# Kernel optimization log

Measured on AMD Instinct MI355X. Metric: run time of the kernel, lower is better.

Reference implementation:

```python
import jax, jax.numpy as jnp
import numpy as np

B, CIN, COUT, CH, H, W = 8, 3, 1, 64, 256, 256
MODES, LAYERS = 4, 6


def conv1x1(x, w, b):
    # x: (B,C,H,W), w: (O,C), b: (O,)
    return jnp.einsum('bchw,oc->bohw', x, w) + b[None, :, None, None]


def koopman(x, w1, w2):
    # FNO-style spectral conv: rfft2 -> truncated-mode complex multiply -> irfft2
    m = MODES
    xf = jnp.fft.rfft2(x)                                    # (B,C,H,W//2+1) complex
    o1 = jnp.einsum('bixy,ioxy->boxy', xf[:, :, :m, :m], w1)
    o2 = jnp.einsum('bixy,ioxy->boxy', xf[:, :, -m:, :m], w2)
    of = jnp.zeros(xf.shape, dtype=xf.dtype)
    of = of.at[:, :, :m, :m].set(o1)
    of = of.at[:, :, -m:, :m].set(o2)
    return jnp.fft.irfft2(of, s=(H, W))


def setup_inputs() -> dict:
    key = jax.random.key(0)
    ks = jax.random.split(key, 12)
    scale = 1.0 / (CH * CH)
    inp = {
        'x': jax.random.normal(ks[0], (B, CIN, H, W), dtype=jnp.float32),
        'enc_w': jax.random.normal(ks[1], (CH, CIN), dtype=jnp.float32) * (1.0 / np.sqrt(CIN)),
        'enc_b': jax.random.normal(ks[2], (CH,), dtype=jnp.float32) * 0.01,
        'dec1_w': jax.random.normal(ks[3], (CH, CH), dtype=jnp.float32) * (1.0 / np.sqrt(CH)),
        'dec1_b': jax.random.normal(ks[4], (CH,), dtype=jnp.float32) * 0.01,
        'dec2_w': jax.random.normal(ks[5], (COUT, CH), dtype=jnp.float32) * (1.0 / np.sqrt(CH)),
        'dec2_b': jax.random.normal(ks[6], (COUT,), dtype=jnp.float32) * 0.01,
        'w1r': jax.random.uniform(ks[7], (CH, CH, MODES, MODES), dtype=jnp.float32) * scale,
        'w1i': jax.random.uniform(ks[8], (CH, CH, MODES, MODES), dtype=jnp.float32) * scale,
        'w2r': jax.random.uniform(ks[9], (CH, CH, MODES, MODES), dtype=jnp.float32) * scale,
        'w2i': jax.random.uniform(ks[10], (CH, CH, MODES, MODES), dtype=jnp.float32) * scale,
    }
    return inp


def reference(x, enc_w, enc_b, dec1_w, dec1_b, dec2_w, dec2_b, w1r, w1i, w2r, w2i):
    w1 = w1r + 1j * w1i
    w2 = w2r + 1j * w2i
    h = jnp.tanh(conv1x1(x, enc_w, enc_b))          # encoder
    skip = h
    for _ in range(LAYERS):                         # fixed small layer count
        h = h + koopman(h, w1, w2)
    h = h + skip
    h = jnp.tanh(conv1x1(h, dec1_w, dec1_b))        # decoder
    return conv1x1(h, dec2_w, dec2_b)
```

## Files before the change

kernel.cpp:

```cpp
#include <hip/hip_runtime.h>
#include <hip/hip_bf16.h>

#define NB 8
#define NCIN 3
#define NCH 64
#define NH 256
#define NW 256
#define NM 4
#define NLAYERS 6

typedef short s16x8 __attribute__((ext_vector_type(8)));
typedef float f32x4 __attribute__((ext_vector_type(4)));

__device__ __forceinline__ float fast_tanh(float x) {
    float e = __expf(2.0f * x);
    return 1.0f - 2.0f * __builtin_amdgcn_rcpf(1.0f + e);
}
__device__ __forceinline__ float sin2pi(float x) { return __builtin_amdgcn_sinf(x); }
__device__ __forceinline__ float cos2pi(float x) { return __builtin_amdgcn_cosf(x); }

__device__ __forceinline__ unsigned int pk2(float a, float b) {
    __hip_bfloat162 h = __float22bfloat162_rn(make_float2(a, b));
    unsigned int u; __builtin_memcpy(&u, &h, 4); return u;
}
__device__ __forceinline__ s16x8 u4cast(uint4 u) {
    s16x8 r; __builtin_memcpy(&r, &u, 16); return r;
}
__device__ __forceinline__ unsigned short f2bf(float f) {
    unsigned int u = __float_as_uint(f);
    u = u + 0x7fffu + ((u >> 16) & 1u);
    return (unsigned short)(u >> 16);
}

__global__ __launch_bounds__(256) void k_prep(
    const float* __restrict__ dec1_w, const float* __restrict__ enc_w,
    const float* __restrict__ enc_b,
    const float* __restrict__ w1r, const float* __restrict__ w1i,
    const float* __restrict__ w2r, const float* __restrict__ w2i,
    unsigned short* __restrict__ Wpk, unsigned short* __restrict__ Tpk,
    float* __restrict__ encwb, float* __restrict__ Wtr, float* __restrict__ Wti,
    float* __restrict__ d1wT)
{
    const int bid = blockIdx.x;
    const int t   = threadIdx.x;
    if (bid < 1024) {
        int elem = bid * 256 + t;
        int ri = elem >> 17;
        int rem = elem & 0x1FFFF;
        int p  = rem >> 14;
        int q  = (rem >> 12) & 3;
        int i  = (rem >> 6) & 63;
        int o  = rem & 63;
        const float* src;
        if (p < 4) src = ri ? w1i : w1r;
        else       src = ri ? w2i : w2r;
        float v = src[((i * 64 + o) * 4 + (p & 3)) * 4 + q];
        float* dst = ri ? Wti : Wtr;
        dst[(p * 4 + q) * 4096 + i * 64 + o] = v;
    } else if (bid < 1026) {
        const int tt = (bid - 1024) * 256 + t;
        const int o  = tt & 63;
        const int cb = (tt >> 6) * 8;
        const float* wr = dec1_w + o * NCH + cb;
        float4 wa = ((const float4*)wr)[0];
        float4 wb = ((const float4*)wr)[1];
        float v[8] = {wa.x, wa.y, wa.z, wa.w, wb.x, wb.y, wb.z, wb.w};
        unsigned int ph[4], pl[4];
        #pragma unroll
        for (int j = 0; j < 4; ++j) {
            unsigned int h = pk2(v[2 * j], v[2 * j + 1]);
            float ha = __uint_as_float(h << 16);
            float hb = __uint_as_float(h & 0xffff0000u);
            ph[j] = h;
            pl[j] = pk2(v[2 * j] - ha, v[2 * j + 1] - hb);
        }
        int byteoff = (o * 128 + cb * 2) ^ ((o & 7) << 4);
        *(uint4*)((char*)Wpk + byteoff)        = make_uint4(ph[0], ph[1], ph[2], ph[3]);
        *(uint4*)((char*)Wpk + 8192 + byteoff) = make_uint4(pl[0], pl[1], pl[2], pl[3]);
    } else if (bid < 1030) {
        const int tt = (bid - 1026) * 256 + t;
        const int n  = tt >> 6;
        const int w4 = (tt & 63) * 4;
        float vv[4];
        #pragma unroll
        for (int z = 0; z < 4; ++z) {
            int w = w4 + z;
            float val = 0.f;
            if (n < 4)      val = cos2pi((float)(n * w) * (1.0f / 256.0f));
            else if (n < 8) val = -sin2pi((float)((n - 4) * w) * (1.0f / 256.0f));
            vv[z] = val;
        }
        *(uint2*)(Tpk + n * 256 + w4) = make_uint2(pk2(vv[0], vv[1]), pk2(vv[2], vv[3]));
    } else if (bid == 1030) {
        if (t < NCH) {
            float4 e4;
            e4.x = enc_w[t * 3 + 0]; e4.y = enc_w[t * 3 + 1];
            e4.z = enc_w[t * 3 + 2]; e4.w = enc_b[t];
            ((float4*)encwb)[t] = e4;
        }
    } else {
        for (int idx = t; idx < 4096; idx += 256) {
            int c = idx >> 6, o = idx & 63;
            d1wT[idx] = dec1_w[o * NCH + c];
        }
    }
}

__global__ __launch_bounds__(256) void k_enc_mfma(
    const float* __restrict__ x, const float* __restrict__ encwb,
    const unsigned short* __restrict__ Tpk, float* __restrict__ P2)
{
    __shared__ __align__(16) unsigned short Ah[64 * 128];
    const int bi  = blockIdx.x;
    const int b   = bi >> 9;
    const int rem = bi & 511;
    const int row = rem >> 1;
    const int wh  = rem & 1;
    const int t   = threadIdx.x;

    {
        const int c   = t & 63;
        const int wl0 = (t >> 6) * 32;
        float4 ewb = ((const float4*)encwb)[c];
        const float* xr0 = x + ((b * 3 + 0) * NH + row) * NW + wh * 128 + wl0;
        const float* xr1 = x + ((b * 3 + 1) * NH + row) * NW + wh * 128 + wl0;
        const float* xr2 = x + ((b * 3 + 2) * NH + row) * NW + wh * 128 + wl0;
        #pragma unroll
        for (int u = 0; u < 4; ++u) {
            float4 a0 = ((const float4*)xr0)[u * 2], b0 = ((const float4*)xr0)[u * 2 + 1];
            float4 a1 = ((const float4*)xr1)[u * 2], b1 = ((const float4*)xr1)[u * 2 + 1];
            float4 a2 = ((const float4*)xr2)[u * 2], b2 = ((const float4*)xr2)[u * 2 + 1];
            float hv[8];
            hv[0] = fast_tanh(ewb.w + ewb.x * a0.x + ewb.y * a1.x + ewb.z * a2.x);
            hv[1] = fast_tanh(ewb.w + ewb.x * a0.y + ewb.y * a1.y + ewb.z * a2.y);
            hv[2] = fast_tanh(ewb.w + ewb.x * a0.z + ewb.y * a1.z + ewb.z * a2.z);
            hv[3] = fast_tanh(ewb.w + ewb.x * a0.w + ewb.y * a1.w + ewb.z * a2.w);
            hv[4] = fast_tanh(ewb.w + ewb.x * b0.x + ewb.y * b1.x + ewb.z * b2.x);
            hv[5] = fast_tanh(ewb.w + ewb.x * b0.y + ewb.y * b1.y + ewb.z * b2.y);
            hv[6] = fast_tanh(ewb.w + ewb.x * b0.z + ewb.y * b1.z + ewb.z * b2.z);
            hv[7] = fast_tanh(ewb.w + ewb.x * b0.w + ewb.y * b1.w + ewb.z * b2.w);
            uint4 pu = make_uint4(pk2(hv[0], hv[1]), pk2(hv[2], hv[3]),
                                  pk2(hv[4], hv[5]), pk2(hv[6], hv[7]));
            int byteoff = (c * 256 + (wl0 + u * 8) * 2) ^ ((c & 15) << 4);
            *(uint4*)((char*)Ah + byteoff) = pu;
        }
    }
    __syncthreads();

    const int lane = t & 63;
    const int v    = t >> 6;
    const int li   = lane & 15;
    const int g    = lane >> 4;
    f32x4 acc = {0.f, 0.f, 0.f, 0.f};
    #pragma unroll
    for (int kk = 0; kk < 4; ++kk) {
        int cm = v * 16 + li;
        int coff = (cm * 256 + (kk * 32 + g * 8) * 2) ^ ((cm & 15) << 4);
        s16x8 ah = *(const s16x8*)((const char*)Ah + coff);
        int wg = wh * 128 + kk * 32 + g * 8;
        s16x8 bh = *(const s16x8*)(Tpk + li * 256 + wg);
        acc = __builtin_amdgcn_mfma_f32_16x16x32_bf16(ah, bh, acc, 0, 0, 0);
    }
    if (li < 8) {
        const int q = li & 3, reim = li >> 2;
        float* pbase = P2 + (size_t)wh * (NB * 64 * 256 * 8);
        #pragma unroll
        for (int e = 0; e < 4; ++e) {
            int c = v * 16 + g * 4 + e;
            pbase[(((b * 64 + c) * 256 + row) * 4 + q) * 2 + reim] = acc[e];
        }
    }
}

__global__ __launch_bounds__(64) void k_coldft(const float* __restrict__ P2,
                                               float2* __restrict__ s0)
{
    __shared__ __align__(16) float Ps[256][8];
    __shared__ float twc[5][256];
    __shared__ float tws[5][256];
    const int b = blockIdx.x >> 6;
    const int c = blockIdx.x & 63;
    const int t = threadIdx.x;
    {
        const float4* pa = (const float4*)(P2 + (size_t)(b * 64 + c) * 256 * 8);
        const float4* pb = pa + (size_t)NB * 64 * 256 * 2;
        float4* ds = (float4*)&Ps[0][0];
        #pragma unroll
        for (int k = 0; k < 8; ++k) {
            int s = t + 64 * k;
            float4 u = pa[s], v = pb[s];
            ds[s] = make_float4(u.x + v.x, u.y + v.y, u.z + v.z, u.w + v.w);
        }
        for (int idx = t; idx < 5 * 256; idx += 64) {
            int k = idx >> 8, rw = idx & 255;
            float a = (float)(k * rw) * (1.0f / 256.0f);
            twc[k][rw] = cos2pi(a);
            tws[k][rw] = sin2pi(a);
        }
    }
    __syncthreads();
    const int kxs[8] = {0, 1, 2, 3, -4, -3, -2, -1};
    const int p = t >> 3, q = (t >> 1) & 3, reim = t & 1;
    const int kx = kxs[p];
    const int ka = kx < 0 ? -kx : kx;
    const float sgn = (kx < 0) ? 1.f : -1.f;
    float acc = 0.f;
    #pragma unroll 4
    for (int rw = 0; rw < 256; ++rw) {
        float pr = Ps[rw][q * 2], pi = Ps[rw][q * 2 + 1];
        float tr = twc[ka][rw], ti = sgn * tws[ka][rw];
        acc += reim ? (pr * ti + pi * tr) : (pr * tr - pi * ti);
    }
    ((float*)s0)[(((b * 8 + p) * 4 + q) * NCH + c) * 2 + reim] = acc;
}

__global__ __launch_bounds__(128) void k_spec(
    const float* __restrict__ Wtr, const float* __restrict__ Wti,
    const float* __restrict__ d1wT, const float2* __restrict__ s0,
    float2* __restrict__ dd2)
{
    __shared__ float Wr[2][NCH * NCH];
    __shared__ float Wi[2][NCH * NCH];
    __shared__ float sr[2][NCH], si[2][NCH];
    __shared__ float2 FL[2][NCH];
    __shared__ float W1T[NCH * NCH];
    const int gx    = blockIdx.x;
    const int b     = gx / 17;
    const int slot  = gx % 17;
    const int which = threadIdx.x >> 6;
    const int o     = threadIdx.x & 63;
    const int tid   = threadIdx.x;

    int p = -1, q = 0, g = -1;
    if (slot < 12) {
        int r = slot * 2 + which;
        q = (r >> 3) + 1;
        p = r & 7;
    } else {
        g = slot - 12;
        if (which == 0) p = g;
        else            p = (g == 1) ? 7 : (g == 2) ? 6 : (g == 3) ? 5 : -1;
        q = 0;
    }
    const bool active = (p >= 0);

    if (active) {
        const float4* wr = (const float4*)(Wtr + (p * 4 + q) * 4096);
        const float4* wi = (const float4*)(Wti + (p * 4 + q) * 4096);
        float4* dr = (float4*)&Wr[which][0];
        float4* di = (float4*)&Wi[which][0];
        #pragma unroll
        for (int k = 0; k < 16; ++k) {
            dr[o + 64 * k] = wr[o + 64 * k];
            di[o + 64 * k] = wi[o + 64 * k];
        }
        float2 sv = s0[((b * 8 + p) * 4 + q) * NCH + o];
        sr[which][o] = sv.x; si[which][o] = sv.y;
    }
    {
        float4* w1 = (float4*)W1T;
        const float4* sw = (const float4*)d1wT;
        #pragma unroll
        for (int k = 0; k < 8; ++k) w1[tid + 128 * k] = sw[tid + 128 * k];
    }
    __syncthreads();

    float dr = 0.f, di = 0.f, d8r = 0.f, d8i = 0.f;
    if (slot < 12) {
        for (int l = 0; l < NLAYERS; ++l) {
            float Fr = 0.f, Fi = 0.f;
            for (int i = 0; i < NCH; ++i) {
                float a0 = sr[which][i], a1 = si[which][i];
                float b0 = Wr[which][i * NCH + o], b1 = Wi[which][i * NCH + o];
                Fr += a0 * b0 - a1 * b1;
                Fi += a0 * b1 + a1 * b0;
            }
            __syncthreads();
            sr[which][o] += Fr; si[which][o] += Fi;
            dr += Fr; di += Fi;
            __syncthreads();
        }
    } else {
        for (int l = 0; l < NLAYERS; ++l) {
            float Fr = 0.f, Fi = 0.f;
            if (active) {
                for (int i = 0; i < NCH; ++i) {
                    float a0 = sr[which][i], a1 = si[which][i];
                    float b0 = Wr[which][i * NCH + o], b1 = Wi[which][i * NCH + o];
                    Fr += a0 * b0 - a1 * b1;
                    Fi += a0 * b1 + a1 * b0;
                }
            }
            FL[which][o] = make_float2(Fr, Fi);
            __syncthreads();
            float addr_ = 0.f, addi_ = 0.f;
            if (active) {
                if (g == 0) { addr_ = Fr; addi_ = 0.f; }
                else if (g == 4) {
                    addr_ = 0.5f * Fr; addi_ = 0.5f * Fi;
                    d8r += 0.5f * Fr;  d8i -= 0.5f * Fi;
                } else {
                    float2 Fo = FL[1 - which][o];
                    addr_ = 0.5f * (Fr + Fo.x);
                    addi_ = 0.5f * (Fi - Fo.y);
                }
                sr[which][o] += addr_; si[which][o] += addi_;
                dr += addr_; di += addi_;
            }
            __syncthreads();
        }
    }

    sr[which][o] = dr; si[which][o] = di;
    if (slot == 16 && which == 0) FL[0][o] = make_float2(d8r, d8i);
    __syncthreads();
    float2* db = dd2 + (size_t)b * (9 * 4 * NCH);
    if (active) {
        float ar = 0.f, ai = 0.f;
        for (int c = 0; c < NCH; ++c) {
            float wv = W1T[c * NCH + o];
            ar += sr[which][c] * wv;
            ai += si[which][c] * wv;
        }
        db[(p * 4 + q) * NCH + o] = make_float2(ar, ai);
    }
    if (slot == 16 && which == 0) {
        float ar = 0.f, ai = 0.f;
        for (int c = 0; c < NCH; ++c) {
            float wv = W1T[c * NCH + o];
            ar += FL[0][c].x * wv;
            ai += FL[0][c].y * wv;
        }
        db[(8 * 4 + 0) * NCH + o] = make_float2(ar, ai);
    }
}

__global__ __launch_bounds__(256) void k_final(
    const float* __restrict__ x, const float* __restrict__ encwb,
    const unsigned short* __restrict__ Wpk, const float2* __restrict__ dd2,
    const float* __restrict__ dec1_b, const float* __restrict__ dec2_w,
    const float* __restrict__ dec2_b, float* __restrict__ out)
{
    __shared__ __align__(16) unsigned short Wl[2][NCH * NCH];
    __shared__ __align__(16) unsigned short BcsT[NCH][8];
    const int bi   = blockIdx.x;
    const int b    = bi >> 9;
    const int rem  = bi & 511;
    const int row  = rem >> 1;
    const int half = rem & 1;
    const int t    = threadIdx.x;

    {
        const uint4* src = (const uint4*)Wpk;
        uint4* dst = (uint4*)&Wl[0][0];
        #pragma unroll
        for (int k = 0; k < 4; ++k) dst[t + 256 * k] = src[t + 256 * k];
    }
    {
        const int o = t & 63;
        const int v = t >> 6;
        float tc[5], ts[5];
        tc[0] = 1.f; ts[0] = 0.f;
        #pragma unroll
        for (int k = 1; k < 5; ++k) {
            float a = (float)(k * row) * (1.0f / 256.0f);
            tc[k] = cos2pi(a); ts[k] = sin2pi(a);
        }
        const float2* dv = dd2 + (size_t)b * (9 * 4 * NCH);
        float twr[9] = {tc[0], tc[1], tc[2], tc[3], tc[4], tc[3], tc[2], tc[1], tc[4]};
        float twi[9] = {ts[0], ts[1], ts[2], ts[3], -ts[4], -ts[3], -ts[2], -ts[1], ts[4]};
        if (v == 0) {
            float gr = 0.f;
            #pragma unroll
            for (int p = 0; p < 9; ++p) {
                float2 u = dv[(p * 4 + 0) * NCH + o];
                gr += u.x * twr[p] - u.y * twi[p];
            }
            BcsT[o][0] = f2bf(gr * (1.0f / 65536.0f));
            BcsT[o][7] = 0;
        } else {
            const int q = v;
            float gr = 0.f, gi = 0.f;
            #pragma unroll
            for (int p = 0; p < 8; ++p) {
                float2 u = dv[(p * 4 + q) * NCH + o];
                gr += u.x * twr[p] - u.y * twi[p];
                gi += u.x * twi[p] + u.y * twr[p];
            }
            BcsT[o][q]     = f2bf(gr * (2.0f / 65536.0f));
            BcsT[o][3 + q] = f2bf(-gi * (2.0f / 65536.0f));
        }
    }
    __syncthreads();

    const int lane = t & 63;
    const int wv   = t >> 6;
    const int li   = lane & 15;
    const int g    = lane >> 4;

    s16x8 ahi[2][2], alo[2][2];
    {
        float xs0[2], xs1[2], xs2[2];
        #pragma unroll
        for (int i = 0; i < 2; ++i) {
            int px = half * 128 + (wv * 2 + i) * 16 + li;
            xs0[i] = x[((b * 3 + 0) * NH + row) * NW + px];
            xs1[i] = x[((b * 3 + 1) * NH + row) * NW + px];
            xs2[i] = x[((b * 3 + 2) * NH + row) * NW + px];
        }
        #pragma unroll
        for (int ks = 0; ks < 2; ++ks) {
            unsigned int hu[2][4], lu[2][4];
            #pragma unroll
            for (int j2 = 0; j2 < 4; ++j2) {
                float4 e0 = ((const float4*)encwb)[ks * 32 + g * 8 + j2 * 2 + 0];
                float4 e1 = ((const float4*)encwb)[ks * 32 + g * 8 + j2 * 2 + 1];
                #pragma unroll
                for (int i = 0; i < 2; ++i) {
                    float va = 2.0f * fast_tanh(e0.w + e0.x * xs0[i] + e0.y * xs1[i] + e0.z * xs2[i]);
                    float vb = 2.0f * fast_tanh(e1.w + e1.x * xs0[i] + e1.y * xs1[i] + e1.z * xs2[i]);
                    unsigned int h = pk2(va, vb);
                    float ha = __uint_as_float(h << 16);
                    float hb = __uint_as_float(h & 0xffff0000u);
                    hu[i][j2] = h;
                    lu[i][j2] = pk2(va - ha, vb - hb);
                }
            }
            #pragma unroll
            for (int i = 0; i < 2; ++i) {
                ahi[i][ks] = u4cast(make_uint4(hu[i][0], hu[i][1], hu[i][2], hu[i][3]));
                alo[i][ks] = u4cast(make_uint4(lu[i][0], lu[i][1], lu[i][2], lu[i][3]));
            }
        }
    }

    f32x4 acc[2][4];
    #pragma unroll
    for (int i = 0; i < 2; ++i)
        #pragma unroll
        for (int nt = 0; nt < 4; ++nt)
            acc[i][nt] = (f32x4){0.f, 0.f, 0.f, 0.f};
    #pragma unroll
    for (int ks = 0; ks < 2; ++ks) {
        #pragma unroll
        for (int nt = 0; nt < 4; ++nt) {
            int o = nt * 16 + li;
            int byteoff = (o * 128 + ks * 64 + g * 16) ^ ((o & 7) << 4);
            s16x8 wh = *(const s16x8*)((const char*)&Wl[0][0] + byteoff);
            s16x8 wl = *(const s16x8*)((const char*)&Wl[1][0] + byteoff);
            #pragma unroll
            for (int i = 0; i < 2; ++i) {
                acc[i][nt] = __builtin_amdgcn_mfma_f32_16x16x32_bf16(ahi[i][ks], wh, acc[i][nt], 0, 0, 0);
                acc[i][nt] = __builtin_amdgcn_mfma_f32_16x16x32_bf16(alo[i][ks], wh, acc[i][nt], 0, 0, 0);
                acc[i][nt] = __builtin_amdgcn_mfma_f32_16x16x32_bf16(ahi[i][ks], wl, acc[i][nt], 0, 0, 0);
            }
        }
    }

    {
        s16x8 aC[2];
        #pragma unroll
        for (int i = 0; i < 2; ++i) {
            if (g == 0) {
                int px = half * 128 + (wv * 2 + i) * 16 + li;
                float pf = (float)px;
                float c1 = cos2pi(pf * (1.0f / 256.0f)), s1 = sin2pi(pf * (1.0f / 256.0f));
                float c2 = cos2pi(pf * (2.0f / 256.0f)), s2 = sin2pi(pf * (2.0f / 256.0f));
                float c3 = cos2pi(pf * (3.0f / 256.0f)), s3 = sin2pi(pf * (3.0f / 256.0f));
                aC[i] = u4cast(make_uint4(pk2(1.0f, c1), pk2(c2, c3),
                                          pk2(s1, s2), pk2(s3, 0.0f)));
            } else {
                aC[i] = u4cast(make_uint4(0, 0, 0, 0));
            }
        }
        #pragma unroll
        for (int nt = 0; nt < 4; ++nt) {
            s16x8 bC;
            if (g == 0) bC = *(const s16x8*)(&BcsT[nt * 16 + li][0]);
            else        bC = u4cast(make_uint4(0, 0, 0, 0));
            #pragma unroll
            for (int i = 0; i < 2; ++i)
                acc[i][nt] = __builtin_amdgcn_mfma_f32_16x16x32_bf16(aC[i], bC, acc[i][nt], 0, 0, 0);
        }
    }

    float d1b[4], d2w[4];
    #pragma unroll
    for (int nt = 0; nt < 4; ++nt) {
        int o = nt * 16 + li;
        d1b[nt] = dec1_b[o];
        d2w[nt] = dec2_w[o];
    }
    const float d2b = dec2_b[0];
    float* orow = out + (b * NH + row) * NW;
    #pragma unroll
    for (int i = 0; i < 2; ++i) {
        #pragma unroll
        for (int r = 0; r < 4; ++r) {
            float partial = 0.f;
            #pragma unroll
            for (int nt = 0; nt < 4; ++nt) {
                float sv = acc[i][nt][r] + d1b[nt];
                partial += d2w[nt] * fast_tanh(sv);
            }
            partial += __shfl_xor(partial, 1);
            partial += __shfl_xor(partial, 2);
            partial += __shfl_xor(partial, 4);
            partial += __shfl_xor(partial, 8);
            if (li == 0) {
                int px = half * 128 + (wv * 2 + i) * 16 + g * 4 + r;
                orow[px] = d2b + partial;
            }
        }
    }
}

extern "C" void kernel_launch(void* const* d_in, const int* in_sizes, int n_in,
                              void* d_out, int out_size, void* d_ws, size_t ws_size,
                              hipStream_t stream) {
    (void)in_sizes; (void)n_in; (void)out_size; (void)ws_size;
    const float* x      = (const float*)d_in[0];
    const float* enc_w  = (const float*)d_in[1];
    const float* enc_b  = (const float*)d_in[2];
    const float* dec1_w = (const float*)d_in[3];
    const float* dec1_b = (const float*)d_in[4];
    const float* dec2_w = (const float*)d_in[5];
    const float* dec2_b = (const float*)d_in[6];
    const float* w1r    = (const float*)d_in[7];
    const float* w1i    = (const float*)d_in[8];
    const float* w2r    = (const float*)d_in[9];
    const float* w2i    = (const float*)d_in[10];
    float* out = (float*)d_out;

    char* ws = (char*)d_ws;
    float*  P2    = (float*)(ws);
    float2* s0    = (float2*)(ws + (8u << 20));
    float2* dd2   = (float2*)(ws + (8u << 20) + 131072);
    char*   p0    = ws + (8u << 20) + 131072 + 147456;
    unsigned short* Wpk = (unsigned short*)(p0);
    unsigned short* Tpk = (unsigned short*)(p0 + 16384);
    float*  encwb = (float*)(p0 + 16384 + 8192);
    float*  Wtr   = (float*)(p0 + 16384 + 8192 + 1024);
    float*  Wti   = (float*)(p0 + 16384 + 8192 + 1024 + 524288);
    float*  d1wT  = (float*)(p0 + 16384 + 8192 + 1024 + 1048576);

    k_prep     <<<1032, 256, 0, stream>>>(dec1_w, enc_w, enc_b, w1r, w1i, w2r, w2i,
                                          Wpk, Tpk, encwb, Wtr, Wti, d1wT);
    k_enc_mfma <<<NB * NH * 2, 256, 0, stream>>>(x, encwb, Tpk, P2);
    k_coldft   <<<NB * NCH, 64, 0, stream>>>(P2, s0);
    k_spec     <<<NB * 17, 128, 0, stream>>>(Wtr, Wti, d1wT, s0, dd2);
    k_final    <<<NB * NH * 2, 256, 0, stream>>>(x, encwb, Wpk, dd2, dec1_b,
                                                 dec2_w, dec2_b, out);
}
```

Measured before the change: 167.4 us.

## Process full rows per block and drop bf16 low-part split in final GEMM

The encoder kernel now handles a whole 256-wide row per block, so the split-half partial spectra buffer and its summation in the column DFT go away. The final kernel runs 512 threads per row instead of two 256-thread half-row blocks, which halves the redundant per-block weight loads and twiddle setup. It also removes the low-order bf16 correction term for the activations, cutting one MFMA per tile at the cost of some accuracy.

```diff
diff --git a/kernel.cpp b/kernel.cpp
--- a/kernel.cpp
+++ b/kernel.cpp
@@ -110,23 +110,21 @@
     const float* __restrict__ x, const float* __restrict__ encwb,
     const unsigned short* __restrict__ Tpk, float* __restrict__ P2)
 {
-    __shared__ __align__(16) unsigned short Ah[64 * 128];
+    __shared__ __align__(16) unsigned short Ah[64 * 256];
     const int bi  = blockIdx.x;
-    const int b   = bi >> 9;
-    const int rem = bi & 511;
-    const int row = rem >> 1;
-    const int wh  = rem & 1;
+    const int b   = bi >> 8;
+    const int row = bi & 255;
     const int t   = threadIdx.x;
 
     {
         const int c   = t & 63;
-        const int wl0 = (t >> 6) * 32;
+        const int wl0 = (t >> 6) * 64;
         float4 ewb = ((const float4*)encwb)[c];
-        const float* xr0 = x + ((b * 3 + 0) * NH + row) * NW + wh * 128 + wl0;
-        const float* xr1 = x + ((b * 3 + 1) * NH + row) * NW + wh * 128 + wl0;
-        const float* xr2 = x + ((b * 3 + 2) * NH + row) * NW + wh * 128 + wl0;
-        #pragma unroll
-        for (int u = 0; u < 4; ++u) {
+        const float* xr0 = x + ((b * 3 + 0) * NH + row) * NW + wl0;
+        const float* xr1 = x + ((b * 3 + 1) * NH + row) * NW + wl0;
+        const float* xr2 = x + ((b * 3 + 2) * NH + row) * NW + wl0;
+        #pragma unroll
+        for (int u = 0; u < 8; ++u) {
             float4 a0 = ((const float4*)xr0)[u * 2], b0 = ((const float4*)xr0)[u * 2 + 1];
             float4 a1 = ((const float4*)xr1)[u * 2], b1 = ((const float4*)xr1)[u * 2 + 1];
             float4 a2 = ((const float4*)xr2)[u * 2], b2 = ((const float4*)xr2)[u * 2 + 1];
@@ -141,7 +139,7 @@
             hv[7] = fast_tanh(ewb.w + ewb.x * b0.w + ewb.y * b1.w + ewb.z * b2.w);
             uint4 pu = make_uint4(pk2(hv[0], hv[1]), pk2(hv[2], hv[3]),
                                   pk2(hv[4], hv[5]), pk2(hv[6], hv[7]));
-            int byteoff = (c * 256 + (wl0 + u * 8) * 2) ^ ((c & 15) << 4);
+            int byteoff = (c * 512 + (wl0 + u * 8) * 2) ^ ((c & 15) << 4);
             *(uint4*)((char*)Ah + byteoff) = pu;
         }
     }
@@ -153,21 +151,20 @@
     const int g    = lane >> 4;
     f32x4 acc = {0.f, 0.f, 0.f, 0.f};
     #pragma unroll
-    for (int kk = 0; kk < 4; ++kk) {
+    for (int kk = 0; kk < 8; ++kk) {
         int cm = v * 16 + li;
-        int coff = (cm * 256 + (kk * 32 + g * 8) * 2) ^ ((cm & 15) << 4);
+        int coff = (cm * 512 + (kk * 32 + g * 8) * 2) ^ ((cm & 15) << 4);
         s16x8 ah = *(const s16x8*)((const char*)Ah + coff);
-        int wg = wh * 128 + kk * 32 + g * 8;
+        int wg = kk * 32 + g * 8;
         s16x8 bh = *(const s16x8*)(Tpk + li * 256 + wg);
         acc = __builtin_amdgcn_mfma_f32_16x16x32_bf16(ah, bh, acc, 0, 0, 0);
     }
     if (li < 8) {
         const int q = li & 3, reim = li >> 2;
-        float* pbase = P2 + (size_t)wh * (NB * 64 * 256 * 8);
         #pragma unroll
         for (int e = 0; e < 4; ++e) {
             int c = v * 16 + g * 4 + e;
-            pbase[(((b * 64 + c) * 256 + row) * 4 + q) * 2 + reim] = acc[e];
+            P2[(((b * 64 + c) * 256 + row) * 4 + q) * 2 + reim] = acc[e];
         }
     }
 }
@@ -183,13 +180,11 @@
     const int t = threadIdx.x;
     {
         const float4* pa = (const float4*)(P2 + (size_t)(b * 64 + c) * 256 * 8);
-        const float4* pb = pa + (size_t)NB * 64 * 256 * 2;
         float4* ds = (float4*)&Ps[0][0];
         #pragma unroll
         for (int k = 0; k < 8; ++k) {
             int s = t + 64 * k;
-            float4 u = pa[s], v = pb[s];
-            ds[s] = make_float4(u.x + v.x, u.y + v.y, u.z + v.z, u.w + v.w);
+            ds[s] = pa[s];
         }
         for (int idx = t; idx < 5 * 256; idx += 64) {
             int k = idx >> 8, rw = idx & 255;
@@ -335,7 +330,7 @@
     }
 }
 
-__global__ __launch_bounds__(256) void k_final(
+__global__ __launch_bounds__(512) void k_final(
     const float* __restrict__ x, const float* __restrict__ encwb,
     const unsigned short* __restrict__ Wpk, const float2* __restrict__ dd2,
     const float* __restrict__ dec1_b, const float* __restrict__ dec2_w,
@@ -344,19 +339,17 @@
     __shared__ __align__(16) unsigned short Wl[2][NCH * NCH];
     __shared__ __align__(16) unsigned short BcsT[NCH][8];
     const int bi   = blockIdx.x;
-    const int b    = bi >> 9;
-    const int rem  = bi & 511;
-    const int row  = rem >> 1;
-    const int half = rem & 1;
+    const int b    = bi >> 8;
+    const int row  = bi & 255;
     const int t    = threadIdx.x;
 
     {
         const uint4* src = (const uint4*)Wpk;
         uint4* dst = (uint4*)&Wl[0][0];
         #pragma unroll
-        for (int k = 0; k < 4; ++k) dst[t + 256 * k] = src[t + 256 * k];
-    }
-    {
+        for (int k = 0; k < 2; ++k) dst[t + 512 * k] = src[t + 512 * k];
+    }
+    if (t < 256) {
         const int o = t & 63;
         const int v = t >> 6;
         float tc[5], ts[5];
@@ -398,19 +391,19 @@
     const int li   = lane & 15;
     const int g    = lane >> 4;
 
-    s16x8 ahi[2][2], alo[2][2];
+    s16x8 ahi[2][2];
     {
         float xs0[2], xs1[2], xs2[2];
         #pragma unroll
         for (int i = 0; i < 2; ++i) {
-            int px = half * 128 + (wv * 2 + i) * 16 + li;
+            int px = (wv * 2 + i) * 16 + li;
             xs0[i] = x[((b * 3 + 0) * NH + row) * NW + px];
             xs1[i] = x[((b * 3 + 1) * NH + row) * NW + px];
             xs2[i] = x[((b * 3 + 2) * NH + row) * NW + px];
         }
         #pragma unroll
         for (int ks = 0; ks < 2; ++ks) {
-            unsigned int hu[2][4], lu[2][4];
+            unsigned int hu[2][4];
             #pragma unroll
             for (int j2 = 0; j2 < 4; ++j2) {
                 float4 e0 = ((const float4*)encwb)[ks * 32 + g * 8 + j2 * 2 + 0];
@@ -419,18 +412,12 @@
                 for (int i = 0; i < 2; ++i) {
                     float va = 2.0f * fast_tanh(e0.w + e0.x * xs0[i] + e0.y * xs1[i] + e0.z * xs2[i]);
                     float vb = 2.0f * fast_tanh(e1.w + e1.x * xs0[i] + e1.y * xs1[i] + e1.z * xs2[i]);
-                    unsigned int h = pk2(va, vb);
-                    float ha = __uint_as_float(h << 16);
-                    float hb = __uint_as_float(h & 0xffff0000u);
-                    hu[i][j2] = h;
-                    lu[i][j2] = pk2(va - ha, vb - hb);
+                    hu[i][j2] = pk2(va, vb);
                 }
             }
             #pragma unroll
-            for (int i = 0; i < 2; ++i) {
+            for (int i = 0; i < 2; ++i)
                 ahi[i][ks] = u4cast(make_uint4(hu[i][0], hu[i][1], hu[i][2], hu[i][3]));
-                alo[i][ks] = u4cast(make_uint4(lu[i][0], lu[i][1], lu[i][2], lu[i][3]));
-            }
         }
     }
 
@@ -451,7 +438,6 @@
             #pragma unroll
             for (int i = 0; i < 2; ++i) {
                 acc[i][nt] = __builtin_amdgcn_mfma_f32_16x16x32_bf16(ahi[i][ks], wh, acc[i][nt], 0, 0, 0);
-                acc[i][nt] = __builtin_amdgcn_mfma_f32_16x16x32_bf16(alo[i][ks], wh, acc[i][nt], 0, 0, 0);
                 acc[i][nt] = __builtin_amdgcn_mfma_f32_16x16x32_bf16(ahi[i][ks], wl, acc[i][nt], 0, 0, 0);
             }
         }
@@ -462,7 +448,7 @@
         #pragma unroll
         for (int i = 0; i < 2; ++i) {
             if (g == 0) {
-                int px = half * 128 + (wv * 2 + i) * 16 + li;
+                int px = (wv * 2 + i) * 16 + li;
                 float pf = (float)px;
                 float c1 = cos2pi(pf * (1.0f / 256.0f)), s1 = sin2pi(pf * (1.0f / 256.0f));
                 float c2 = cos2pi(pf * (2.0f / 256.0f)), s2 = sin2pi(pf * (2.0f / 256.0f));
@@ -508,7 +494,7 @@
             partial += __shfl_xor(partial, 4);
             partial += __shfl_xor(partial, 8);
             if (li == 0) {
-                int px = half * 128 + (wv * 2 + i) * 16 + g * 4 + r;
+                int px = (wv * 2 + i) * 16 + g * 4 + r;
                 orow[px] = d2b + partial;
             }
         }
@@ -534,9 +520,9 @@
 
     char* ws = (char*)d_ws;
     float*  P2    = (float*)(ws);
-    float2* s0    = (float2*)(ws + (8u << 20));
-    float2* dd2   = (float2*)(ws + (8u << 20) + 131072);
-    char*   p0    = ws + (8u << 20) + 131072 + 147456;
+    float2* s0    = (float2*)(ws + (4u << 20));
+    float2* dd2   = (float2*)(ws + (4u << 20) + 131072);
+    char*   p0    = ws + (4u << 20) + 131072 + 147456;
     unsigned short* Wpk = (unsigned short*)(p0);
     unsigned short* Tpk = (unsigned short*)(p0 + 16384);
     float*  encwb = (float*)(p0 + 16384 + 8192);
@@ -546,9 +532,9 @@
 
     k_prep     <<<1032, 256, 0, stream>>>(dec1_w, enc_w, enc_b, w1r, w1i, w2r, w2i,
                                           Wpk, Tpk, encwb, Wtr, Wti, d1wT);
-    k_enc_mfma <<<NB * NH * 2, 256, 0, stream>>>(x, encwb, Tpk, P2);
+    k_enc_mfma <<<NB * NH, 256, 0, stream>>>(x, encwb, Tpk, P2);
     k_coldft   <<<NB * NCH, 64, 0, stream>>>(P2, s0);
     k_spec     <<<NB * 17, 128, 0, stream>>>(Wtr, Wti, d1wT, s0, dd2);
-    k_final    <<<NB * NH * 2, 256, 0, stream>>>(x, encwb, Wpk, dd2, dec1_b,
-                                                 dec2_w, dec2_b, out);
-}
+    k_final    <<<NB * NH, 512, 0, stream>>>(x, encwb, Wpk, dd2, dec1_b,
+                                             dec2_w, dec2_b, out);
+}
```

Result: faster. 162.3 us (-3.1%).
